# Kernel optimization log

Hardware: AMD Instinct MI355X
Metric: run time of the kernel (lower is better)

## Reference

```python
import jax, jax.numpy as jnp
import numpy as np

D = 1024
H = 16
DH = D // H

def setup_inputs() -> dict:
    key = jax.random.key(0)
    k1, k2, k3, k4 = jax.random.split(key, 4)
    x = jax.random.normal(k1, (4, 2048, D), dtype=jnp.float32)
    # qkv_linear: Linear(D, D, bias=False); weight stored as (out, in) torch-style
    w_qkv = jax.random.normal(k2, (D, D), dtype=jnp.float32) * (1.0 / np.sqrt(D))
    # final linear: Linear(D, D) with bias
    w_out = jax.random.normal(k3, (D, D), dtype=jnp.float32) * (1.0 / np.sqrt(D))
    b_out = jax.random.normal(k4, (D,), dtype=jnp.float32) * 0.01
    return {"x": x, "w_qkv": w_qkv, "w_out": w_out, "b_out": b_out}

def reference(x, w_qkv, w_out, b_out):
    B, S, E = x.shape
    # Same projection used for Q, K, V (faithful to original module)
    qkv = jnp.einsum('bse,de->bsd', x, w_qkv)           # [B,S,D]
    qkv = qkv.reshape(B, S, H, DH).transpose(0, 2, 1, 3)  # [B,H,S,Dh]
    q = k = v = qkv
    scale = DH ** -0.5
    attn = jnp.einsum('bhqd,bhkd->bhqk', q, k) * scale   # [B,H,S,S]
    attn = jax.nn.softmax(attn, axis=-1)
    out = jnp.einsum('bhqk,bhkd->bhqd', attn, v)         # [B,H,S,Dh]
    out = out.transpose(0, 2, 1, 3).reshape(B, S, E)
    return jnp.einsum('bse,de->bsd', out, w_out) + b_out
```

## Files before the change

### kernel.cpp

```cpp
#include <hip/hip_runtime.h>
#include <hip/hip_bf16.h>
#include <stdint.h>

typedef unsigned short u16;
typedef unsigned int   u32;
typedef unsigned long long u64;
typedef __bf16 bf16x8 __attribute__((ext_vector_type(8)));
typedef float  f32x4  __attribute__((ext_vector_type(4)));

#define D_MODEL 1024
#define NH 16
#define DHEAD 64
#define BB 4
#define SS 2048
#define MM (BB*SS)

__device__ __forceinline__ u16 f2bf(float f) {
    unsigned int u = __float_as_uint(f);
    u += 0x7fffu + ((u >> 16) & 1u);
    return (u16)(u >> 16);
}
__device__ __forceinline__ float bf2f(u16 s) {
    return __uint_as_float(((unsigned int)s) << 16);
}
__device__ __forceinline__ u32 pkbf(float a, float b) {
    __hip_bfloat162 h = __float22bfloat162_rn(make_float2(a, b));
    return *(u32*)&h;
}

union U8 {
    uint4 q;
    u16   v[8];
    bf16x8 f;
};

#define N4X (MM * D_MODEL / 4)
#define N4W (D_MODEL * D_MODEL / 4)
__global__ __launch_bounds__(256) void cvt_all_kernel(const float* __restrict__ x,
                                                      const float* __restrict__ wq,
                                                      const float* __restrict__ wo,
                                                      u16* __restrict__ xb,
                                                      u16* __restrict__ wqb,
                                                      u16* __restrict__ wob) {
    int i = blockIdx.x * 256 + threadIdx.x;
    const float* s; u16* d; int off;
    if (i < N4X)            { s = x;  d = xb;  off = i; }
    else if (i < N4X + N4W) { s = wq; d = wqb; off = i - N4X; }
    else                    { s = wo; d = wob; off = i - N4X - N4W; }
    float4 f = ((const float4*)s)[off];
    u32 o[2] = { pkbf(f.x, f.y), pkbf(f.z, f.w) };
    ((uint2*)d)[off] = *(const uint2*)o;
}

template <bool PERMUTE_OUT>
__device__ __forceinline__ void gemm_body(const u16* __restrict__ A,
                                          const u16* __restrict__ Bt,
                                          const float* __restrict__ Bo,
                                          u16* __restrict__ Cq, u16* __restrict__ CqT,
                                          float* __restrict__ Out)
{
    __shared__ __align__(16) u16 As[128*64];
    __shared__ __align__(16) u16 Bs[128*64];

    const int tid  = threadIdx.x;
    const int wave = tid >> 6;
    const int lane = tid & 63;
    const int quad = lane >> 4;
    const int l16  = lane & 15;
    const int bm = blockIdx.x >> 3;
    const int bn = blockIdx.x & 7;
    const int wm = wave >> 1, wn = wave & 1;

    f32x4 acc[4][4] = {};

    const int rp = tid >> 3;
    const int ch = tid & 7;
    const int sc = ch ^ (rp & 7);

    const u16* Ab = A  + (size_t)(bm * 128 + rp) * D_MODEL + sc * 8;
    const u16* Bb = Bt + (size_t)(bn * 128 + rp) * D_MODEL + sc * 8;
    const int xr = l16 & 7;

    for (int k0 = 0; k0 < D_MODEL; k0 += 64) {
#pragma unroll
        for (int p = 0; p < 4; ++p) {
            __builtin_amdgcn_global_load_lds(
                (__attribute__((address_space(1))) void*)(Ab + (size_t)(32*p) * D_MODEL + k0),
                (__attribute__((address_space(3))) void*)(As + p*2048 + tid*8), 16, 0, 0);
            __builtin_amdgcn_global_load_lds(
                (__attribute__((address_space(1))) void*)(Bb + (size_t)(32*p) * D_MODEL + k0),
                (__attribute__((address_space(3))) void*)(Bs + p*2048 + tid*8), 16, 0, 0);
        }
        __syncthreads();

#pragma unroll
        for (int ks = 0; ks < 2; ++ks) {
            bf16x8 af[4], bfr[4];
#pragma unroll
            for (int t = 0; t < 4; ++t)
                af[t] = *(const bf16x8*)(const void*)(
                    As + (wm*64 + t*16 + l16)*64 + (((ks*4 + quad) ^ xr) * 8));
#pragma unroll
            for (int t = 0; t < 4; ++t)
                bfr[t] = *(const bf16x8*)(const void*)(
                    Bs + (wn*64 + t*16 + l16)*64 + (((ks*4 + quad) ^ xr) * 8));
#pragma unroll
            for (int i = 0; i < 4; ++i)
#pragma unroll
                for (int j = 0; j < 4; ++j)
                    acc[i][j] = __builtin_amdgcn_mfma_f32_16x16x32_bf16(af[i], bfr[j], acc[i][j], 0, 0, 0);
        }
        __syncthreads();
    }

    const int rowbase = bm*128 + wm*64;
    const int colbase = bn*128 + wn*64;
    if (PERMUTE_OUT) {
#pragma unroll
        for (int j = 0; j < 4; ++j) {
            const int col = colbase + j*16 + l16;
            const int h = col >> 6, dh = col & 63;
#pragma unroll
            for (int i = 0; i < 4; ++i) {
                const int row0 = rowbase + i*16 + quad*4;
                const int b = row0 >> 11, s0 = row0 & (SS - 1);
#pragma unroll
                for (int r = 0; r < 4; ++r)
                    Cq[(((size_t)(b*NH + h))*SS + s0 + r)*DHEAD + dh] = f2bf(acc[i][j][r]);
                u64 w = (u64)pkbf(acc[i][j][0], acc[i][j][1])
                      | ((u64)pkbf(acc[i][j][2], acc[i][j][3]) << 32);
                *(u64*)(CqT + ((size_t)((b*NH + h)*DHEAD + dh))*SS + s0) = w;
            }
        }
    } else {
#pragma unroll
        for (int j = 0; j < 4; ++j) {
            const int col = colbase + j*16 + l16;
            const float bias = Bo[col];
#pragma unroll
            for (int i = 0; i < 4; ++i) {
#pragma unroll
                for (int r = 0; r < 4; ++r) {
                    const int row = rowbase + i*16 + quad*4 + r;
                    Out[(size_t)row * D_MODEL + col] = acc[i][j][r] + bias;
                }
            }
        }
    }
}

__global__ __launch_bounds__(256) void gemm_qkv_kernel(const u16* __restrict__ A,
                                                       const u16* __restrict__ Bt,
                                                       u16* __restrict__ Cq,
                                                       u16* __restrict__ CqT) {
    gemm_body<true>(A, Bt, nullptr, Cq, CqT, nullptr);
}

__global__ __launch_bounds__(256) void gemm_out_kernel(const u16* __restrict__ A,
                                                       const u16* __restrict__ Bt,
                                                       const float* __restrict__ Bo,
                                                       float* __restrict__ Out) {
    gemm_body<false>(A, Bt, Bo, nullptr, nullptr, Out);
}

__global__ __launch_bounds__(256, 4) void attn_kernel(const u16* __restrict__ qkv,
                                                      const u16* __restrict__ qkvT,
                                                      u16* __restrict__ outb)
{
    __shared__ __align__(16) u16 Ks[2*2048];
    __shared__ __align__(16) u16 Vt[2*2048];
    __shared__ __align__(16) u16 Pl[4*1280];

    const int tid  = threadIdx.x;
    const int wave = tid >> 6;
    const int lane = tid & 63;
    const int quad = lane >> 4;
    const int l16  = lane & 15;

    const int bh   = blockIdx.x >> 4;
    const int qblk = blockIdx.x & 15;
    const int b = bh >> 4, h = bh & 15;
    const int qbase = qblk * 128 + wave * 32;

    const u16* Qp = qkv + (size_t)bh * SS * DHEAD;
    const float qscale = 0.125f * 1.4426950408889634f;

    bf16x8 qb[2][2];
#pragma unroll
    for (int nt = 0; nt < 2; ++nt)
#pragma unroll
        for (int ks = 0; ks < 2; ++ks) {
            U8 raw; raw.q = *(const uint4*)(Qp + (size_t)(qbase + nt*16 + l16)*DHEAD + ks*32 + quad*8);
            U8 w;
#pragma unroll
            for (int jj = 0; jj < 4; ++jj)
                ((u32*)&w)[jj] = pkbf(bf2f(raw.v[2*jj]) * qscale, bf2f(raw.v[2*jj+1]) * qscale);
            qb[nt][ks] = w.f;
        }

    const int rK = tid >> 3, cK = (tid & 7) ^ ((rK >> 1) & 7);
    const u16* srcK = qkv  + (size_t)bh * SS * DHEAD + rK * DHEAD + cK * 8;
    const int rV = tid >> 2, cV = (tid & 3) ^ ((rV >> 1) & 3);
    const u16* srcV = qkvT + (size_t)bh * DHEAD * SS + (size_t)rV * SS + cV * 8;

    const int h8 = (l16 >> 1) & 7, h4 = (l16 >> 1) & 3;
    const int ko0 = l16*64 + ((quad)     ^ h8) * 8;
    const int ko1 = l16*64 + ((4 + quad) ^ h8) * 8;
    const int vo  = l16*32 + ((quad) ^ h4) * 8;

    u16* Pw       = Pl + wave*1280 + l16*40 + quad*4;
    const u16* Pr = Pl + wave*1280 + l16*40 + quad*8;

    bf16x8 ones;
#pragma unroll
    for (int j = 0; j < 8; ++j) ones[j] = (__bf16)1.0f;

    f32x4 ot[4][2] = {};
    f32x4 lsum[2]  = {};

    __builtin_amdgcn_global_load_lds(
        (__attribute__((address_space(1))) void*)(srcK),
        (__attribute__((address_space(3))) void*)(Ks + tid*8), 16, 0, 0);
    __builtin_amdgcn_global_load_lds(
        (__attribute__((address_space(1))) void*)(srcV),
        (__attribute__((address_space(3))) void*)(Vt + tid*8), 16, 0, 0);

#pragma unroll 2
    for (int kt = 0; kt < SS/32; ++kt) {
        __syncthreads();
        if (kt < SS/32 - 1) {
            __builtin_amdgcn_global_load_lds(
                (__attribute__((address_space(1))) void*)(srcK + (size_t)(kt+1)*32*DHEAD),
                (__attribute__((address_space(3))) void*)(Ks + ((kt+1)&1)*2048 + tid*8), 16, 0, 0);
            __builtin_amdgcn_global_load_lds(
                (__attribute__((address_space(1))) void*)(srcV + (kt+1)*32),
                (__attribute__((address_space(3))) void*)(Vt + ((kt+1)&1)*2048 + tid*8), 16, 0, 0);
        }
        const u16* Kb = Ks + (kt&1)*2048;
        const u16* Vb = Vt + (kt&1)*2048;

#pragma unroll
        for (int mt = 0; mt < 2; ++mt) {
            f32x4 s[2] = {};
            bf16x8 kf0 = *(const bf16x8*)(const void*)(Kb + mt*1024 + ko0);
            bf16x8 kf1 = *(const bf16x8*)(const void*)(Kb + mt*1024 + ko1);
#pragma unroll
            for (int nt = 0; nt < 2; ++nt)
                s[nt] = __builtin_amdgcn_mfma_f32_16x16x32_bf16(kf0, qb[nt][0], s[nt], 0, 0, 0);
#pragma unroll
            for (int nt = 0; nt < 2; ++nt)
                s[nt] = __builtin_amdgcn_mfma_f32_16x16x32_bf16(kf1, qb[nt][1], s[nt], 0, 0, 0);
#pragma unroll
            for (int nt = 0; nt < 2; ++nt) {
                float p0 = __builtin_amdgcn_exp2f(s[nt][0]);
                float p1 = __builtin_amdgcn_exp2f(s[nt][1]);
                float p2 = __builtin_amdgcn_exp2f(s[nt][2]);
                float p3 = __builtin_amdgcn_exp2f(s[nt][3]);
                u64 w = (u64)pkbf(p0, p1) | ((u64)pkbf(p2, p3) << 32);
                *(u64*)(Pw + nt*640 + mt*16) = w;
            }
        }

        bf16x8 pf[2];
#pragma unroll
        for (int nt = 0; nt < 2; ++nt)
            pf[nt] = *(const bf16x8*)(const void*)(Pr + nt*640);
#pragma unroll
        for (int nt = 0; nt < 2; ++nt)
            lsum[nt] = __builtin_amdgcn_mfma_f32_16x16x32_bf16(ones, pf[nt], lsum[nt], 0, 0, 0);
        bf16x8 vf[4];
#pragma unroll
        for (int dt = 0; dt < 4; ++dt)
            vf[dt] = *(const bf16x8*)(const void*)(Vb + dt*512 + vo);
#pragma unroll
        for (int dt = 0; dt < 4; ++dt)
#pragma unroll
            for (int nt = 0; nt < 2; ++nt)
                ot[dt][nt] = __builtin_amdgcn_mfma_f32_16x16x32_bf16(vf[dt], pf[nt], ot[dt][nt], 0, 0, 0);
    }

    float inv[2];
#pragma unroll
    for (int nt = 0; nt < 2; ++nt) inv[nt] = 1.0f / lsum[nt][0];
#pragma unroll
    for (int dt = 0; dt < 4; ++dt)
#pragma unroll
        for (int nt = 0; nt < 2; ++nt) {
            u64 w = (u64)pkbf(ot[dt][nt][0]*inv[nt], ot[dt][nt][1]*inv[nt])
                  | ((u64)pkbf(ot[dt][nt][2]*inv[nt], ot[dt][nt][3]*inv[nt]) << 32);
            *(u64*)(outb + ((size_t)(b*SS + qbase + nt*16 + l16))*D_MODEL
                         + h*64 + dt*16 + quad*4) = w;
        }
}

extern "C" void kernel_launch(void* const* d_in, const int* in_sizes, int n_in,
                              void* d_out, int out_size, void* d_ws, size_t ws_size,
                              hipStream_t stream)
{
    (void)in_sizes; (void)n_in; (void)out_size; (void)ws_size;
    const float* x  = (const float*)d_in[0];
    const float* wq = (const float*)d_in[1];
    const float* wo = (const float*)d_in[2];
    const float* bo = (const float*)d_in[3];

    char* ws = (char*)d_ws;
    u16* xb    = (u16*)(ws);
    u16* wqb   = (u16*)(ws + (size_t)(16 << 20));
    u16* wob   = (u16*)(ws + (size_t)(18 << 20));
    u16* qkvb  = (u16*)(ws + (size_t)(20 << 20));
    u16* qkvTb = (u16*)(ws + (size_t)(36 << 20));
    u16* attb  = xb;

    cvt_all_kernel<<<(N4X + 2*N4W) / 256, 256, 0, stream>>>(x, wq, wo, xb, wqb, wob);
    gemm_qkv_kernel<<<(MM/128) * (D_MODEL/128), 256, 0, stream>>>(xb, wqb, qkvb, qkvTb);
    attn_kernel<<<BB * NH * (SS/128), 256, 0, stream>>>(qkvb, qkvTb, attb);
    gemm_out_kernel<<<(MM/128) * (D_MODEL/128), 256, 0, stream>>>(attb, wob, bo, (float*)d_out);
}
```

Measured before the change: 236.8 us.

## Keep softmax P in registers using 16x16x16 MFMA, halve attention block size

Drops the LDS round-trip for the probability tile. The exp2 results are packed straight into registers and fed to 16x16x16 bf16 MFMAs, whose input layout matches the QK^T output layout, for both the row-sum and the PV product. The attention block shrinks to 2 waves and 64 queries, so each thread now issues two K/V tile loads and the grid doubles. In exchange the kernel runs twice as many smaller MFMAs, and each K/V tile loaded into LDS is reused by fewer query rows.

Measured after the change: 251.4 us. 6.2% more time.

```diff
diff --git a/kernel.cpp b/kernel.cpp
--- a/kernel.cpp
+++ b/kernel.cpp
@@ -6,6 +6,7 @@
 typedef unsigned int   u32;
 typedef unsigned long long u64;
 typedef __bf16 bf16x8 __attribute__((ext_vector_type(8)));
+typedef short  s16x4  __attribute__((ext_vector_type(4)));
 typedef float  f32x4  __attribute__((ext_vector_type(4)));
 
 #define D_MODEL 1024
@@ -163,13 +164,12 @@
     gemm_body<false>(A, Bt, Bo, nullptr, nullptr, Out);
 }
 
-__global__ __launch_bounds__(256, 4) void attn_kernel(const u16* __restrict__ qkv,
+__global__ __launch_bounds__(128, 4) void attn_kernel(const u16* __restrict__ qkv,
                                                       const u16* __restrict__ qkvT,
                                                       u16* __restrict__ outb)
 {
     __shared__ __align__(16) u16 Ks[2*2048];
     __shared__ __align__(16) u16 Vt[2*2048];
-    __shared__ __align__(16) u16 Pl[4*1280];
 
     const int tid  = threadIdx.x;
     const int wave = tid >> 6;
@@ -177,10 +177,10 @@
     const int quad = lane >> 4;
     const int l16  = lane & 15;
 
-    const int bh   = blockIdx.x >> 4;
-    const int qblk = blockIdx.x & 15;
+    const int bh   = blockIdx.x >> 5;
+    const int qblk = blockIdx.x & 31;
     const int b = bh >> 4, h = bh & 15;
-    const int qbase = qblk * 128 + wave * 32;
+    const int qbase = qblk * 64 + wave * 32;
 
     const u16* Qp = qkv + (size_t)bh * SS * DHEAD;
     const float qscale = 0.125f * 1.4426950408889634f;
@@ -198,47 +198,57 @@
             qb[nt][ks] = w.f;
         }
 
-    const int rK = tid >> 3, cK = (tid & 7) ^ ((rK >> 1) & 7);
+    const int rK = tid >> 3;
+    const int cK = (tid & 7) ^ ((rK >> 1) & 7);
     const u16* srcK = qkv  + (size_t)bh * SS * DHEAD + rK * DHEAD + cK * 8;
-    const int rV = tid >> 2, cV = (tid & 3) ^ ((rV >> 1) & 3);
+    const int rV = tid >> 2;
+    const int cV = (tid & 3) ^ ((rV >> 1) & 3);
     const u16* srcV = qkvT + (size_t)bh * DHEAD * SS + (size_t)rV * SS + cV * 8;
 
     const int h8 = (l16 >> 1) & 7, h4 = (l16 >> 1) & 3;
     const int ko0 = l16*64 + ((quad)     ^ h8) * 8;
     const int ko1 = l16*64 + ((4 + quad) ^ h8) * 8;
-    const int vo  = l16*32 + ((quad) ^ h4) * 8;
-
-    u16* Pw       = Pl + wave*1280 + l16*40 + quad*4;
-    const u16* Pr = Pl + wave*1280 + l16*40 + quad*8;
-
-    bf16x8 ones;
-#pragma unroll
-    for (int j = 0; j < 8; ++j) ones[j] = (__bf16)1.0f;
+    int vo[2];
+#pragma unroll
+    for (int kk = 0; kk < 2; ++kk)
+        vo[kk] = l16*32 + (((kk*2 + (quad >> 1)) ^ h4) * 8) + (quad & 1)*4;
+
+    s16x4 ones4;
+#pragma unroll
+    for (int j = 0; j < 4; ++j) ones4[j] = (short)0x3F80;
 
     f32x4 ot[4][2] = {};
     f32x4 lsum[2]  = {};
 
-    __builtin_amdgcn_global_load_lds(
-        (__attribute__((address_space(1))) void*)(srcK),
-        (__attribute__((address_space(3))) void*)(Ks + tid*8), 16, 0, 0);
-    __builtin_amdgcn_global_load_lds(
-        (__attribute__((address_space(1))) void*)(srcV),
-        (__attribute__((address_space(3))) void*)(Vt + tid*8), 16, 0, 0);
+#pragma unroll
+    for (int p = 0; p < 2; ++p) {
+        __builtin_amdgcn_global_load_lds(
+            (__attribute__((address_space(1))) void*)(srcK + p*16*DHEAD),
+            (__attribute__((address_space(3))) void*)(Ks + p*1024 + tid*8), 16, 0, 0);
+        __builtin_amdgcn_global_load_lds(
+            (__attribute__((address_space(1))) void*)(srcV + (size_t)p*32*SS),
+            (__attribute__((address_space(3))) void*)(Vt + p*1024 + tid*8), 16, 0, 0);
+    }
 
 #pragma unroll 2
     for (int kt = 0; kt < SS/32; ++kt) {
         __syncthreads();
         if (kt < SS/32 - 1) {
-            __builtin_amdgcn_global_load_lds(
-                (__attribute__((address_space(1))) void*)(srcK + (size_t)(kt+1)*32*DHEAD),
-                (__attribute__((address_space(3))) void*)(Ks + ((kt+1)&1)*2048 + tid*8), 16, 0, 0);
-            __builtin_amdgcn_global_load_lds(
-                (__attribute__((address_space(1))) void*)(srcV + (kt+1)*32),
-                (__attribute__((address_space(3))) void*)(Vt + ((kt+1)&1)*2048 + tid*8), 16, 0, 0);
+            const int bo = ((kt+1)&1) * 2048;
+#pragma unroll
+            for (int p = 0; p < 2; ++p) {
+                __builtin_amdgcn_global_load_lds(
+                    (__attribute__((address_space(1))) void*)(srcK + (size_t)((kt+1)*32 + p*16)*DHEAD),
+                    (__attribute__((address_space(3))) void*)(Ks + bo + p*1024 + tid*8), 16, 0, 0);
+                __builtin_amdgcn_global_load_lds(
+                    (__attribute__((address_space(1))) void*)(srcV + (kt+1)*32 + (size_t)p*32*SS),
+                    (__attribute__((address_space(3))) void*)(Vt + bo + p*1024 + tid*8), 16, 0, 0);
+            }
         }
         const u16* Kb = Ks + (kt&1)*2048;
         const u16* Vb = Vt + (kt&1)*2048;
 
+        s16x4 pf[2][2];
 #pragma unroll
         for (int mt = 0; mt < 2; ++mt) {
             f32x4 s[2] = {};
@@ -252,31 +262,29 @@
                 s[nt] = __builtin_amdgcn_mfma_f32_16x16x32_bf16(kf1, qb[nt][1], s[nt], 0, 0, 0);
 #pragma unroll
             for (int nt = 0; nt < 2; ++nt) {
-                float p0 = __builtin_amdgcn_exp2f(s[nt][0]);
-                float p1 = __builtin_amdgcn_exp2f(s[nt][1]);
-                float p2 = __builtin_amdgcn_exp2f(s[nt][2]);
-                float p3 = __builtin_amdgcn_exp2f(s[nt][3]);
-                u64 w = (u64)pkbf(p0, p1) | ((u64)pkbf(p2, p3) << 32);
-                *(u64*)(Pw + nt*640 + mt*16) = w;
-            }
-        }
-
-        bf16x8 pf[2];
-#pragma unroll
-        for (int nt = 0; nt < 2; ++nt)
-            pf[nt] = *(const bf16x8*)(const void*)(Pr + nt*640);
-#pragma unroll
-        for (int nt = 0; nt < 2; ++nt)
-            lsum[nt] = __builtin_amdgcn_mfma_f32_16x16x32_bf16(ones, pf[nt], lsum[nt], 0, 0, 0);
-        bf16x8 vf[4];
-#pragma unroll
-        for (int dt = 0; dt < 4; ++dt)
-            vf[dt] = *(const bf16x8*)(const void*)(Vb + dt*512 + vo);
-#pragma unroll
-        for (int dt = 0; dt < 4; ++dt)
+                u32 lo = pkbf(__builtin_amdgcn_exp2f(s[nt][0]), __builtin_amdgcn_exp2f(s[nt][1]));
+                u32 hi = pkbf(__builtin_amdgcn_exp2f(s[nt][2]), __builtin_amdgcn_exp2f(s[nt][3]));
+                ((u32*)&pf[mt][nt])[0] = lo;
+                ((u32*)&pf[mt][nt])[1] = hi;
+            }
+        }
+
+#pragma unroll
+        for (int mt = 0; mt < 2; ++mt)
 #pragma unroll
             for (int nt = 0; nt < 2; ++nt)
-                ot[dt][nt] = __builtin_amdgcn_mfma_f32_16x16x32_bf16(vf[dt], pf[nt], ot[dt][nt], 0, 0, 0);
+                lsum[nt] = __builtin_amdgcn_mfma_f32_16x16x16bf16_1k(ones4, pf[mt][nt], lsum[nt], 0, 0, 0);
+
+#pragma unroll
+        for (int dt = 0; dt < 4; ++dt) {
+#pragma unroll
+            for (int kk = 0; kk < 2; ++kk) {
+                s16x4 vf = *(const s16x4*)(const void*)(Vb + dt*512 + vo[kk]);
+#pragma unroll
+                for (int nt = 0; nt < 2; ++nt)
+                    ot[dt][nt] = __builtin_amdgcn_mfma_f32_16x16x16bf16_1k(vf, pf[kk][nt], ot[dt][nt], 0, 0, 0);
+            }
+        }
     }
 
     float inv[2];
@@ -313,6 +321,6 @@
 
     cvt_all_kernel<<<(N4X + 2*N4W) / 256, 256, 0, stream>>>(x, wq, wo, xb, wqb, wob);
     gemm_qkv_kernel<<<(MM/128) * (D_MODEL/128), 256, 0, stream>>>(xb, wqb, qkvb, qkvTb);
-    attn_kernel<<<BB * NH * (SS/128), 256, 0, stream>>>(qkvb, qkvTb, attb);
+    attn_kernel<<<BB * NH * (SS/64), 128, 0, stream>>>(qkvb, qkvTb, attb);
     gemm_out_kernel<<<(MM/128) * (D_MODEL/128), 256, 0, stream>>>(attb, wob, bo, (float*)d_out);
 }
```
